# Kernel optimization log

Hardware: AMD Instinct MI355X
Metric: run time of the kernel (lower is better)

## Reference

```python
import jax, jax.numpy as jnp
import numpy as np

INNER_D = 4096
LORA_RANK = 2
LORA_ALPHA = 1.0
BATCH, SEQ = 4, 4096


def setup_inputs() -> dict:
    key = jax.random.key(0)
    k_x, k_aq, k_bq, k_as, k_bs = jax.random.split(key, 5)
    x_in = jax.random.normal(k_x, (BATCH, SEQ, INNER_D), dtype=jnp.float32)
    # bnb int8 quantized LoRA weights (row-major [out, in], as nn.Linear stores)
    a_q = jax.random.randint(k_aq, (LORA_RANK, INNER_D), -127, 128, dtype=jnp.int8)
    b_q = jax.random.randint(k_bq, (INNER_D, LORA_RANK), -127, 128, dtype=jnp.int8)
    # per-output-row dequant scales (absmax/127), small positive values
    a_scale = jax.random.uniform(k_as, (LORA_RANK,), jnp.float32, 0.005, 0.02)
    b_scale = jax.random.uniform(k_bs, (INNER_D,), jnp.float32, 0.005, 0.02)
    return {"x_in": x_in, "a_q": a_q, "a_scale": a_scale, "b_q": b_q, "b_scale": b_scale}


def reference(x_in, a_q, a_scale, b_q, b_scale):
    scale = LORA_ALPHA / LORA_RANK  # lora_alpha / lora_rank = 0.5
    # inline dequantization: int8 weight * per-row scale
    A = a_q.astype(jnp.float32) * a_scale[:, None]   # [rank, d]
    B = b_q.astype(jnp.float32) * b_scale[:, None]   # [d, rank]
    h = jnp.einsum('bsd,rd->bsr', x_in, A)           # lora_a(x)
    out = scale * jnp.einsum('bsr,dr->bsd', h, B)    # (alpha/rank) * lora_b(h)
    return out
```

## Files before the change

kernel.cpp:

```cpp
#include <hip/hip_runtime.h>
#include <hip/hip_bf16.h>


#define QL_D    4096
#define QL_ROWS 16384
#define K1_ROWS 4
#define K2_ROWS 8

__global__ __launch_bounds__(256) void qlora_h_kernel(
    const float* __restrict__ x,
    const int*   __restrict__ a_q,
    const float* __restrict__ a_scale,
    float2*      __restrict__ h_out)
{
    const int t    = threadIdx.x;
    const int row0 = blockIdx.x * K1_ROWS;

    float fa0[16], fa1[16];
    const int4* a0p = (const int4*)a_q;
    const int4* a1p = (const int4*)(a_q + QL_D);
#pragma unroll
    for (int k = 0; k < 4; ++k) {
        const int4 q0 = a0p[t + 256 * k];
        const int4 q1 = a1p[t + 256 * k];
        fa0[4*k+0] = (float)q0.x; fa0[4*k+1] = (float)q0.y;
        fa0[4*k+2] = (float)q0.z; fa0[4*k+3] = (float)q0.w;
        fa1[4*k+0] = (float)q1.x; fa1[4*k+1] = (float)q1.y;
        fa1[4*k+2] = (float)q1.z; fa1[4*k+3] = (float)q1.w;
    }

    __shared__ float s0[K1_ROWS][4], s1[K1_ROWS][4];
    const int wave = t >> 6;
    const int lane = t & 63;

    const float4* x4 = (const float4*)(x + (size_t)row0 * QL_D);

#pragma unroll
    for (int r = 0; r < K1_ROWS; ++r) {
        float h0 = 0.0f, h1 = 0.0f;
#pragma unroll
        for (int k = 0; k < 4; ++k) {
            const float4 xv = x4[r * (QL_D / 4) + t + 256 * k];
            h0 += xv.x * fa0[4*k+0] + xv.y * fa0[4*k+1]
                + xv.z * fa0[4*k+2] + xv.w * fa0[4*k+3];
            h1 += xv.x * fa1[4*k+0] + xv.y * fa1[4*k+1]
                + xv.z * fa1[4*k+2] + xv.w * fa1[4*k+3];
        }
#pragma unroll
        for (int off = 32; off > 0; off >>= 1) {
            h0 += __shfl_down(h0, off, 64);
            h1 += __shfl_down(h1, off, 64);
        }
        if (lane == 0) { s0[r][wave] = h0; s1[r][wave] = h1; }
    }
    __syncthreads();

    if (t < K1_ROWS) {
        const float H0 = (s0[t][0] + s0[t][1] + s0[t][2] + s0[t][3]) * a_scale[0];
        const float H1 = (s1[t][0] + s1[t][1] + s1[t][2] + s1[t][3]) * a_scale[1];
        h_out[row0 + t] = make_float2(H0, H1);
    }
}

__global__ __launch_bounds__(256) void qlora_out_kernel(
    const float2* __restrict__ h_in,
    const int*    __restrict__ b_q,
    const float*  __restrict__ b_scale,
    float*        __restrict__ out)
{
    const int t    = threadIdx.x;
    const int row0 = blockIdx.x * K2_ROWS;

    float bb0[16], bb1[16];
    const int4*   bq4 = (const int4*)b_q;
    const float4* bs4 = (const float4*)b_scale;
#pragma unroll
    for (int k = 0; k < 4; ++k) {
        const int d4 = t + 256 * k;
        const float4 bs = bs4[d4];
        const int4   q0 = bq4[2 * d4];
        const int4   q1 = bq4[2 * d4 + 1];
        bb0[4*k+0] = 0.5f * bs.x * (float)q0.x; bb1[4*k+0] = 0.5f * bs.x * (float)q0.y;
        bb0[4*k+1] = 0.5f * bs.y * (float)q0.z; bb1[4*k+1] = 0.5f * bs.y * (float)q0.w;
        bb0[4*k+2] = 0.5f * bs.z * (float)q1.x; bb1[4*k+2] = 0.5f * bs.z * (float)q1.y;
        bb0[4*k+3] = 0.5f * bs.w * (float)q1.z; bb1[4*k+3] = 0.5f * bs.w * (float)q1.w;
    }

    float4* o4 = (float4*)(out + (size_t)row0 * QL_D);

#pragma unroll 2
    for (int r = 0; r < K2_ROWS; ++r) {
        const float2 h = h_in[row0 + r];
#pragma unroll
        for (int k = 0; k < 4; ++k) {
            float4 o;
            o.x = h.x * bb0[4*k+0] + h.y * bb1[4*k+0];
            o.y = h.x * bb0[4*k+1] + h.y * bb1[4*k+1];
            o.z = h.x * bb0[4*k+2] + h.y * bb1[4*k+2];
            o.w = h.x * bb0[4*k+3] + h.y * bb1[4*k+3];
            o4[r * (QL_D / 4) + t + 256 * k] = o;
        }
    }
}

extern "C" void kernel_launch(void* const* d_in, const int* in_sizes, int n_in,
                              void* d_out, int out_size, void* d_ws, size_t ws_size,
                              hipStream_t stream) {
    const float* x       = (const float*)d_in[0];
    const int*   a_q     = (const int*)d_in[1];
    const float* a_scale = (const float*)d_in[2];
    const int*   b_q     = (const int*)d_in[3];
    const float* b_scale = (const float*)d_in[4];
    float*       out     = (float*)d_out;
    float2*      h_ws    = (float2*)d_ws;

    qlora_h_kernel  <<<QL_ROWS / K1_ROWS, 256, 0, stream>>>(x, a_q, a_scale, h_ws);
    qlora_out_kernel<<<QL_ROWS / K2_ROWS, 256, 0, stream>>>(h_ws, b_q, b_scale, out);
}
```

Baseline: 451.2 us.

## Fuse LoRA down and up projections into one kernel with nontemporal IO

```diff
diff --git a/kernel.cpp b/kernel.cpp
--- a/kernel.cpp
+++ b/kernel.cpp
@@ -1,46 +1,52 @@
 #include <hip/hip_runtime.h>
-#include <hip/hip_bf16.h>
 
 
 #define QL_D    4096
 #define QL_ROWS 16384
-#define K1_ROWS 4
-#define K2_ROWS 8
+#define RPB     8
 
-__global__ __launch_bounds__(256) void qlora_h_kernel(
+typedef float f32x4 __attribute__((ext_vector_type(4)));
+
+__global__ __launch_bounds__(256) void qlora_fused_kernel(
     const float* __restrict__ x,
     const int*   __restrict__ a_q,
     const float* __restrict__ a_scale,
-    float2*      __restrict__ h_out)
+    const int*   __restrict__ b_q,
+    const float* __restrict__ b_scale,
+    float*       __restrict__ out)
 {
     const int t    = threadIdx.x;
-    const int row0 = blockIdx.x * K1_ROWS;
-
-    float fa0[16], fa1[16];
-    const int4* a0p = (const int4*)a_q;
-    const int4* a1p = (const int4*)(a_q + QL_D);
-#pragma unroll
-    for (int k = 0; k < 4; ++k) {
-        const int4 q0 = a0p[t + 256 * k];
-        const int4 q1 = a1p[t + 256 * k];
-        fa0[4*k+0] = (float)q0.x; fa0[4*k+1] = (float)q0.y;
-        fa0[4*k+2] = (float)q0.z; fa0[4*k+3] = (float)q0.w;
-        fa1[4*k+0] = (float)q1.x; fa1[4*k+1] = (float)q1.y;
-        fa1[4*k+2] = (float)q1.z; fa1[4*k+3] = (float)q1.w;
-    }
-
-    __shared__ float s0[K1_ROWS][4], s1[K1_ROWS][4];
+    const int row0 = blockIdx.x * RPB;
     const int wave = t >> 6;
     const int lane = t & 63;
 
-    const float4* x4 = (const float4*)(x + (size_t)row0 * QL_D);
+    float fa0[16], fa1[16];
+    {
+        const int4* a0p = (const int4*)a_q;
+        const int4* a1p = (const int4*)(a_q + QL_D);
+#pragma unroll
+        for (int k = 0; k < 4; ++k) {
+            const int4 q0 = a0p[t + 256 * k];
+            const int4 q1 = a1p[t + 256 * k];
+            fa0[4*k+0] = (float)q0.x; fa0[4*k+1] = (float)q0.y;
+            fa0[4*k+2] = (float)q0.z; fa0[4*k+3] = (float)q0.w;
+            fa1[4*k+0] = (float)q1.x; fa1[4*k+1] = (float)q1.y;
+            fa1[4*k+2] = (float)q1.z; fa1[4*k+3] = (float)q1.w;
+        }
+    }
+
+    __shared__ float sh0[RPB][4], sh1[RPB][4];
+
+    const f32x4* x4 = (const f32x4*)(x + (size_t)row0 * QL_D);
+    f32x4*       o4 = (f32x4*)(out + (size_t)row0 * QL_D);
 
 #pragma unroll
-    for (int r = 0; r < K1_ROWS; ++r) {
+    for (int r = 0; r < RPB; ++r) {
         float h0 = 0.0f, h1 = 0.0f;
 #pragma unroll
         for (int k = 0; k < 4; ++k) {
-            const float4 xv = x4[r * (QL_D / 4) + t + 256 * k];
+            const f32x4 xv =
+                __builtin_nontemporal_load(&x4[r * (QL_D / 4) + t + 256 * k]);
             h0 += xv.x * fa0[4*k+0] + xv.y * fa0[4*k+1]
                 + xv.z * fa0[4*k+2] + xv.w * fa0[4*k+3];
             h1 += xv.x * fa1[4*k+0] + xv.y * fa1[4*k+1]
@@ -51,54 +57,48 @@
             h0 += __shfl_down(h0, off, 64);
             h1 += __shfl_down(h1, off, 64);
         }
-        if (lane == 0) { s0[r][wave] = h0; s1[r][wave] = h1; }
+        if (lane == 0) { sh0[r][wave] = h0; sh1[r][wave] = h1; }
+    }
+
+    float bb0[16], bb1[16];
+    {
+        const int4*   bq4 = (const int4*)b_q;
+        const float4* bs4 = (const float4*)b_scale;
+#pragma unroll
+        for (int k = 0; k < 4; ++k) {
+            const int d4 = t + 256 * k;
+            const float4 bs = bs4[d4];
+            const int4   q0 = bq4[2 * d4];
+            const int4   q1 = bq4[2 * d4 + 1];
+            bb0[4*k+0] = 0.5f * bs.x * (float)q0.x; bb1[4*k+0] = 0.5f * bs.x * (float)q0.y;
+            bb0[4*k+1] = 0.5f * bs.y * (float)q0.z; bb1[4*k+1] = 0.5f * bs.y * (float)q0.w;
+            bb0[4*k+2] = 0.5f * bs.z * (float)q1.x; bb1[4*k+2] = 0.5f * bs.z * (float)q1.y;
+            bb0[4*k+3] = 0.5f * bs.w * (float)q1.z; bb1[4*k+3] = 0.5f * bs.w * (float)q1.w;
+        }
+    }
+
+    __syncthreads();
+
+    if (t < RPB) {
+        const float H0 = (sh0[t][0] + sh0[t][1] + sh0[t][2] + sh0[t][3]) * a_scale[0];
+        const float H1 = (sh1[t][0] + sh1[t][1] + sh1[t][2] + sh1[t][3]) * a_scale[1];
+        sh0[t][0] = H0;
+        sh1[t][0] = H1;
     }
     __syncthreads();
 
-    if (t < K1_ROWS) {
-        const float H0 = (s0[t][0] + s0[t][1] + s0[t][2] + s0[t][3]) * a_scale[0];
-        const float H1 = (s1[t][0] + s1[t][1] + s1[t][2] + s1[t][3]) * a_scale[1];
-        h_out[row0 + t] = make_float2(H0, H1);
-    }
-}
-
-__global__ __launch_bounds__(256) void qlora_out_kernel(
-    const float2* __restrict__ h_in,
-    const int*    __restrict__ b_q,
-    const float*  __restrict__ b_scale,
-    float*        __restrict__ out)
-{
-    const int t    = threadIdx.x;
-    const int row0 = blockIdx.x * K2_ROWS;
-
-    float bb0[16], bb1[16];
-    const int4*   bq4 = (const int4*)b_q;
-    const float4* bs4 = (const float4*)b_scale;
 #pragma unroll
-    for (int k = 0; k < 4; ++k) {
-        const int d4 = t + 256 * k;
-        const float4 bs = bs4[d4];
-        const int4   q0 = bq4[2 * d4];
-        const int4   q1 = bq4[2 * d4 + 1];
-        bb0[4*k+0] = 0.5f * bs.x * (float)q0.x; bb1[4*k+0] = 0.5f * bs.x * (float)q0.y;
-        bb0[4*k+1] = 0.5f * bs.y * (float)q0.z; bb1[4*k+1] = 0.5f * bs.y * (float)q0.w;
-        bb0[4*k+2] = 0.5f * bs.z * (float)q1.x; bb1[4*k+2] = 0.5f * bs.z * (float)q1.y;
-        bb0[4*k+3] = 0.5f * bs.w * (float)q1.z; bb1[4*k+3] = 0.5f * bs.w * (float)q1.w;
-    }
-
-    float4* o4 = (float4*)(out + (size_t)row0 * QL_D);
-
-#pragma unroll 2
-    for (int r = 0; r < K2_ROWS; ++r) {
-        const float2 h = h_in[row0 + r];
+    for (int r = 0; r < RPB; ++r) {
+        const float H0 = sh0[r][0];
+        const float H1 = sh1[r][0];
 #pragma unroll
         for (int k = 0; k < 4; ++k) {
-            float4 o;
-            o.x = h.x * bb0[4*k+0] + h.y * bb1[4*k+0];
-            o.y = h.x * bb0[4*k+1] + h.y * bb1[4*k+1];
-            o.z = h.x * bb0[4*k+2] + h.y * bb1[4*k+2];
-            o.w = h.x * bb0[4*k+3] + h.y * bb1[4*k+3];
-            o4[r * (QL_D / 4) + t + 256 * k] = o;
+            f32x4 o;
+            o.x = H0 * bb0[4*k+0] + H1 * bb1[4*k+0];
+            o.y = H0 * bb0[4*k+1] + H1 * bb1[4*k+1];
+            o.z = H0 * bb0[4*k+2] + H1 * bb1[4*k+2];
+            o.w = H0 * bb0[4*k+3] + H1 * bb1[4*k+3];
+            __builtin_nontemporal_store(o, &o4[r * (QL_D / 4) + t + 256 * k]);
         }
     }
 }
@@ -112,8 +112,7 @@
     const int*   b_q     = (const int*)d_in[3];
     const float* b_scale = (const float*)d_in[4];
     float*       out     = (float*)d_out;
-    float2*      h_ws    = (float2*)d_ws;
 
-    qlora_h_kernel  <<<QL_ROWS / K1_ROWS, 256, 0, stream>>>(x, a_q, a_scale, h_ws);
-    qlora_out_kernel<<<QL_ROWS / K2_ROWS, 256, 0, stream>>>(h_ws, b_q, b_scale, out);
+    qlora_fused_kernel<<<QL_ROWS / RPB, 256, 0, stream>>>(
+        x, a_q, a_scale, b_q, b_scale, out);
 }
```

Measured after the change: 431.6 us. 1.05x faster.
